# Performance work log

Hardware: AMD Instinct MI355X
Metric: run time of the kernel (lower is better)

## Reference

```python
import jax, jax.numpy as jnp
import numpy as np
from jax import lax

# Model dims (see init_kwargs / mamba_ssm defaults)
B_, L_, D_IN = 8, 512, 128
D_MODEL, N_LAYERS = 512, 2
EXPAND, D_STATE, D_CONV = 2, 16, 4
D_INNER = EXPAND * D_MODEL          # 1024
DT_RANK = (D_MODEL + 15) // 16      # 32


def setup_inputs() -> dict:
    key = jax.random.key(0)
    ks = iter(jax.random.split(key, 32))
    def p(shape, scale=0.02):
        return jax.random.normal(next(ks), shape, jnp.float32) * scale
    inp = {}
    inp["x"] = jax.random.normal(next(ks), (B_, L_, D_IN), jnp.float32)
    # input projection (Linear(input_dim, d_model), with bias)
    inp["proj_in_w"] = p((D_MODEL, D_IN))
    inp["proj_in_b"] = p((D_MODEL,))
    # stacked per-layer Mamba params (leading dim = N_LAYERS)
    inp["in_proj_w"] = p((N_LAYERS, 2 * D_INNER, D_MODEL))      # no bias (mamba default)
    inp["conv_w"]    = p((N_LAYERS, D_INNER, D_CONV))           # depthwise conv1d
    inp["conv_b"]    = p((N_LAYERS, D_INNER))
    inp["x_proj_w"]  = p((N_LAYERS, DT_RANK + 2 * D_STATE, D_INNER))
    inp["dt_proj_w"] = p((N_LAYERS, D_INNER, DT_RANK))
    inp["dt_proj_b"] = jnp.full((N_LAYERS, D_INNER), 0.1, jnp.float32)
    inp["A_log"]     = jnp.log(jnp.tile(jnp.arange(1, D_STATE + 1, dtype=jnp.float32), (N_LAYERS, D_INNER, 1)))
    inp["Dm"]        = jnp.ones((N_LAYERS, D_INNER), jnp.float32)
    inp["out_proj_w"] = p((N_LAYERS, D_MODEL, D_INNER))         # no bias
    # classifier head: Linear(d_model, 64) -> ReLU -> Linear(64, 1)
    inp["cls_w1"] = p((64, D_MODEL)); inp["cls_b1"] = p((64,))
    inp["cls_w2"] = p((1, 64));       inp["cls_b2"] = p((1,))
    return inp


def _mamba_block(h, in_w, cw, cb, xp_w, dt_w, dt_b, A_log, Dm, out_w):
    B, L, _ = h.shape
    xz = jnp.einsum('bld,ed->ble', h, in_w)           # (B, L, 2*d_inner)
    xi, z = jnp.split(xz, 2, axis=-1)
    # causal depthwise conv1d (pad left d_conv-1, crop to L)
    xc = xi.transpose(0, 2, 1)                         # (B, d_inner, L)
    xc = lax.conv_general_dilated(
        xc, cw[:, None, :], (1,), [(D_CONV - 1, 0)],
        feature_group_count=D_INNER,
        dimension_numbers=('NCH', 'OIH', 'NCH')) + cb[None, :, None]
    xc = jax.nn.silu(xc).transpose(0, 2, 1)            # (B, L, d_inner)
    x_dbl = jnp.einsum('bld,ed->ble', xc, xp_w)        # (B, L, dt_rank + 2*d_state)
    dt, Bm, Cm = jnp.split(x_dbl, [DT_RANK, DT_RANK + D_STATE], axis=-1)
    dt = jax.nn.softplus(jnp.einsum('blr,dr->bld', dt, dt_w) + dt_b)  # (B, L, d_inner)
    A = -jnp.exp(A_log)                                # (d_inner, d_state)

    def step(hst, ins):
        dt_t, B_t, C_t, x_t = ins                      # (B,di),(B,ds),(B,ds),(B,di)
        dA = jnp.exp(dt_t[..., None] * A)              # (B, di, ds)
        hst = dA * hst + (dt_t * x_t)[..., None] * B_t[:, None, :]
        y = jnp.einsum('bds,bs->bd', hst, C_t)
        return hst, y

    h0 = jnp.zeros((B, D_INNER, D_STATE), h.dtype)
    xs = (dt.transpose(1, 0, 2), Bm.transpose(1, 0, 2),
          Cm.transpose(1, 0, 2), xc.transpose(1, 0, 2))
    _, ys = lax.scan(step, h0, xs)                     # ys: (L, B, d_inner)
    y = ys.transpose(1, 0, 2) + xc * Dm                # skip term D*x
    y = y * jax.nn.silu(z)                             # gate
    return jnp.einsum('ble,de->bld', y, out_w)         # (B, L, d_model)


def reference(x, proj_in_w, proj_in_b, in_proj_w, conv_w, conv_b, x_proj_w,
              dt_proj_w, dt_proj_b, A_log, Dm, out_proj_w,
              cls_w1, cls_b1, cls_w2, cls_b2):
    h = jnp.einsum('bli,di->bld', x, proj_in_w) + proj_in_b
    for l in range(N_LAYERS):
        h = _mamba_block(h, in_proj_w[l], conv_w[l], conv_b[l], x_proj_w[l],
                         dt_proj_w[l], dt_proj_b[l], A_log[l], Dm[l], out_proj_w[l])
    h = h.mean(axis=1)                                 # (B, d_model); dropout = identity (eval)
    h = jax.nn.relu(h @ cls_w1.T + cls_b1)
    logits = (h @ cls_w2.T + cls_b2).squeeze(-1)       # (B,)
    return logits
```

## Files before the change

### kernel.cpp

```cpp
#include <hip/hip_runtime.h>
#include <hip/hip_bf16.h>

#define B_   8
#define L_   512
#define DIN  128
#define DM   512
#define NLAY 2
#define DI   1024
#define DS   16
#define DTR  32
#define BL   (B_ * L_)
#define KS   8
#define CL   64

typedef short bf16x8 __attribute__((ext_vector_type(8)));
typedef float floatx4 __attribute__((ext_vector_type(4)));

__device__ __forceinline__ unsigned short f2bf(float f) {
    unsigned int u = __float_as_uint(f);
    unsigned int r = (u + 0x7FFF + ((u >> 16) & 1)) >> 16;
    return (unsigned short)r;
}

__global__ __launch_bounds__(256) void cvt_all(
    const float* __restrict__ x,  unsigned short* __restrict__ xbf,
    const float* __restrict__ pw, unsigned short* __restrict__ wpin,
    const float* __restrict__ iw, unsigned short* __restrict__ win,
    const float* __restrict__ ow, unsigned short* __restrict__ wout)
{
    int bid = blockIdx.x;
    const float* src; unsigned short* dst; int off;
    if      (bid < 256)  { src = x;  dst = xbf;  off = bid; }
    else if (bid < 288)  { src = pw; dst = wpin; off = bid - 256; }
    else if (bid < 1312) { src = iw; dst = win;  off = bid - 288; }
    else                 { src = ow; dst = wout; off = bid - 1312; }
    int i = (off * 256 + threadIdx.x) * 8;
    float4 a = *(const float4*)(src + i);
    float4 b = *(const float4*)(src + i + 4);
    unsigned short o[8];
    o[0] = f2bf(a.x); o[1] = f2bf(a.y); o[2] = f2bf(a.z); o[3] = f2bf(a.w);
    o[4] = f2bf(b.x); o[5] = f2bf(b.y); o[6] = f2bf(b.z); o[7] = f2bf(b.w);
    *(uint4*)(dst + i) = *(uint4*)o;
}

__global__ __launch_bounds__(256) void gemm_mfma(
    const unsigned short* __restrict__ A,
    const unsigned short* __restrict__ W,
    const float* __restrict__ bias,
    float* __restrict__ C, unsigned short* __restrict__ Cb,
    int N, int K)
{
    __shared__ unsigned short As[128 * 40];
    __shared__ unsigned short Ws[128 * 40];

    const int tid  = threadIdx.x;
    const int row  = tid >> 1;
    const int half = tid & 1;
    const long aBase = (long)(blockIdx.y * 128 + row) * K + half * 16;
    const long wBase = (long)(blockIdx.x * 128 + row) * K + half * 16;
    const int  lbase = row * 40 + half * 16;

    const int lane = tid & 63;
    const int wv   = tid >> 6;
    const int wm   = (wv >> 1) * 64;
    const int wn   = (wv & 1) * 64;
    const int lr   = lane & 15;
    const int q    = lane >> 4;

    floatx4 acc[4][4];
#pragma unroll
    for (int i = 0; i < 4; ++i)
#pragma unroll
        for (int j = 0; j < 4; ++j)
#pragma unroll
            for (int r = 0; r < 4; ++r) acc[i][j][r] = 0.f;

    for (int k0 = 0; k0 < K; k0 += 32) {
        __syncthreads();
        const unsigned short* ap = A + aBase + k0;
        const unsigned short* wp = W + wBase + k0;
        uint4 a0 = *(const uint4*)ap;
        uint4 a1 = *(const uint4*)(ap + 8);
        uint4 w0 = *(const uint4*)wp;
        uint4 w1 = *(const uint4*)(wp + 8);
        *(uint4*)(As + lbase)     = a0;
        *(uint4*)(As + lbase + 8) = a1;
        *(uint4*)(Ws + lbase)     = w0;
        *(uint4*)(Ws + lbase + 8) = w1;
        __syncthreads();

        bf16x8 af[4], bfr[4];
#pragma unroll
        for (int i = 0; i < 4; ++i)
            af[i] = *(const bf16x8*)(As + (wm + i * 16 + lr) * 40 + q * 8);
#pragma unroll
        for (int j = 0; j < 4; ++j)
            bfr[j] = *(const bf16x8*)(Ws + (wn + j * 16 + lr) * 40 + q * 8);
#pragma unroll
        for (int i = 0; i < 4; ++i)
#pragma unroll
            for (int j = 0; j < 4; ++j)
                acc[i][j] = __builtin_amdgcn_mfma_f32_16x16x32_bf16(
                    af[i], bfr[j], acc[i][j], 0, 0, 0);
    }

#pragma unroll
    for (int i = 0; i < 4; ++i) {
#pragma unroll
        for (int r = 0; r < 4; ++r) {
            const int  crow = blockIdx.y * 128 + wm + i * 16 + q * 4 + r;
            const long base = (long)crow * N + blockIdx.x * 128 + wn + lr;
#pragma unroll
            for (int j = 0; j < 4; ++j) {
                float v = acc[i][j][r];
                C[base + j * 16] = v;
                if (Cb) Cb[base + j * 16] = f2bf(v);
            }
        }
    }
}

__global__ __launch_bounds__(256) void gemm_mfma_n64(
    const unsigned short* __restrict__ A,
    const unsigned short* __restrict__ W,
    const float* __restrict__ bias,
    float* __restrict__ C, unsigned short* __restrict__ Cb,
    int N, int K)
{
    __shared__ unsigned short As[128 * 40];
    __shared__ unsigned short Ws[64 * 40];

    const int tid   = threadIdx.x;
    const int arow  = tid >> 1;
    const int ahalf = tid & 1;
    const long aBase = (long)(blockIdx.y * 128 + arow) * K + ahalf * 16;
    const int  albase = arow * 40 + ahalf * 16;
    const int wrow = tid >> 2;
    const int wq   = tid & 3;
    const long wBase = (long)(blockIdx.x * 64 + wrow) * K + wq * 8;
    const int  wlbase = wrow * 40 + wq * 8;

    const int lane = tid & 63;
    const int wv   = tid >> 6;
    const int wm   = wv * 32;
    const int lr   = lane & 15;
    const int q    = lane >> 4;

    floatx4 acc[2][4];
#pragma unroll
    for (int i = 0; i < 2; ++i)
#pragma unroll
        for (int j = 0; j < 4; ++j)
#pragma unroll
            for (int r = 0; r < 4; ++r) acc[i][j][r] = 0.f;

    for (int k0 = 0; k0 < K; k0 += 32) {
        __syncthreads();
        const unsigned short* ap = A + aBase + k0;
        uint4 a0 = *(const uint4*)ap;
        uint4 a1 = *(const uint4*)(ap + 8);
        uint4 w0 = *(const uint4*)(W + wBase + k0);
        *(uint4*)(As + albase)     = a0;
        *(uint4*)(As + albase + 8) = a1;
        *(uint4*)(Ws + wlbase)     = w0;
        __syncthreads();

        bf16x8 af[2], bfr[4];
#pragma unroll
        for (int i = 0; i < 2; ++i)
            af[i] = *(const bf16x8*)(As + (wm + i * 16 + lr) * 40 + q * 8);
#pragma unroll
        for (int j = 0; j < 4; ++j)
            bfr[j] = *(const bf16x8*)(Ws + (j * 16 + lr) * 40 + q * 8);
#pragma unroll
        for (int i = 0; i < 2; ++i)
#pragma unroll
            for (int j = 0; j < 4; ++j)
                acc[i][j] = __builtin_amdgcn_mfma_f32_16x16x32_bf16(
                    af[i], bfr[j], acc[i][j], 0, 0, 0);
    }

    float bj[4] = {0.f, 0.f, 0.f, 0.f};
    if (bias) {
#pragma unroll
        for (int j = 0; j < 4; ++j)
            bj[j] = bias[blockIdx.x * 64 + j * 16 + lr];
    }
#pragma unroll
    for (int i = 0; i < 2; ++i) {
#pragma unroll
        for (int r = 0; r < 4; ++r) {
            const int  crow = blockIdx.y * 128 + wm + i * 16 + q * 4 + r;
            const long base = (long)crow * N + blockIdx.x * 64 + lr;
#pragma unroll
            for (int j = 0; j < 4; ++j) {
                float v = acc[i][j][r] + bj[j];
                C[base + j * 16] = v;
                if (Cb) Cb[base + j * 16] = f2bf(v);
            }
        }
    }
}

__global__ __launch_bounds__(256) void xproj_partial(
    const float* __restrict__ A, const float* __restrict__ W,
    float* __restrict__ P)
{
    __shared__ float As[16][68];
    __shared__ float Ws[16][68];

    const int tid  = threadIdx.x;
    const int tx   = tid & 15;
    const int ty   = tid >> 4;
    const int lrow = tid >> 2;
    const int lk   = (tid & 3) << 2;
    const int kbase = blockIdx.x * (DI / KS);

    const float* Ap = A + (blockIdx.y * 64 + lrow) * DI + kbase + lk;
    const float* Wp = W + lrow * DI + kbase + lk;

    float acc[4][4] = {};

    for (int k0 = 0; k0 < DI / KS; k0 += 16) {
        float4 av = *(const float4*)(Ap + k0);
        float4 wv = *(const float4*)(Wp + k0);
        __syncthreads();
        As[lk + 0][lrow] = av.x; As[lk + 1][lrow] = av.y;
        As[lk + 2][lrow] = av.z; As[lk + 3][lrow] = av.w;
        Ws[lk + 0][lrow] = wv.x; Ws[lk + 1][lrow] = wv.y;
        Ws[lk + 2][lrow] = wv.z; Ws[lk + 3][lrow] = wv.w;
        __syncthreads();
#pragma unroll
        for (int k = 0; k < 16; ++k) {
            const float4 a4 = *(const float4*)&As[k][ty << 2];
            const float4 w4 = *(const float4*)&Ws[k][tx << 2];
            acc[0][0] += a4.x * w4.x; acc[0][1] += a4.x * w4.y;
            acc[0][2] += a4.x * w4.z; acc[0][3] += a4.x * w4.w;
            acc[1][0] += a4.y * w4.x; acc[1][1] += a4.y * w4.y;
            acc[1][2] += a4.y * w4.z; acc[1][3] += a4.y * w4.w;
            acc[2][0] += a4.z * w4.x; acc[2][1] += a4.z * w4.y;
            acc[2][2] += a4.z * w4.z; acc[2][3] += a4.z * w4.w;
            acc[3][0] += a4.w * w4.x; acc[3][1] += a4.w * w4.y;
            acc[3][2] += a4.w * w4.z; acc[3][3] += a4.w * w4.w;
        }
    }

    float* out = P + (long)blockIdx.x * (BL * 64)
               + (blockIdx.y * 64 + (ty << 2)) * 64 + (tx << 2);
#pragma unroll
    for (int i = 0; i < 4; ++i)
        *(float4*)(out + i * 64) = make_float4(acc[i][0], acc[i][1],
                                               acc[i][2], acc[i][3]);
}

__global__ __launch_bounds__(256) void xproj_reduce(
    const float* __restrict__ P, float* __restrict__ xdbl)
{
    int i = (blockIdx.x * 256 + threadIdx.x) * 4;
    float4 s = *(const float4*)(P + i);
#pragma unroll
    for (int k = 1; k < KS; ++k) {
        float4 p = *(const float4*)(P + (long)k * (BL * 64) + i);
        s.x += p.x; s.y += p.y; s.z += p.z; s.w += p.w;
    }
    *(float4*)(xdbl + i) = s;
}

__global__ __launch_bounds__(256) void conv_silu(
    const float* __restrict__ xz, const float* __restrict__ cw,
    const float* __restrict__ cb, float* __restrict__ xc)
{
    int idx = blockIdx.x * 256 + threadIdx.x;
    int d  = idx & (DI - 1);
    int bl = idx >> 10;
    int t  = bl & (L_ - 1);
    int base = (bl - t) * (2 * DI) + d;
    float acc = cb[d];
    const float* w = cw + d * 4;
    if (t >= 3) {
        acc += w[0] * xz[base + (t - 3) * (2 * DI)];
        acc += w[1] * xz[base + (t - 2) * (2 * DI)];
        acc += w[2] * xz[base + (t - 1) * (2 * DI)];
        acc += w[3] * xz[base + t * (2 * DI)];
    } else {
#pragma unroll
        for (int j = 0; j < 4; ++j) {
            int tt = t - 3 + j;
            if (tt >= 0) acc += w[j] * xz[base + tt * (2 * DI)];
        }
    }
    xc[idx] = acc / (1.f + __expf(-acc));
}

template <int CTRL>
__device__ __forceinline__ float dpp_shr_add(float v) {
    int sh = __builtin_amdgcn_update_dpp(0, __float_as_int(v), CTRL, 0xF, 0xF, true);
    return v + __int_as_float(sh);
}

__global__ __launch_bounds__(256) void scan_fused(
    const float* __restrict__ xc, const float* __restrict__ xdbl,
    const float* __restrict__ A_log, const float* __restrict__ dtw,
    const float* __restrict__ dtpb, const float* __restrict__ Dm,
    const float* __restrict__ xz, unsigned short* __restrict__ ysb16)
{
    __shared__ float  sdtw[16][36];
    __shared__ float  sxd [CL][36];
    __shared__ float2 sdx [CL][17];
    __shared__ float2 sbc [CL][17];
    __shared__ float  sy  [16][68];

    const int tid  = threadIdx.x;
    const int s    = tid & 15;
    const int grp  = tid >> 4;
    const int bd0  = blockIdx.x * 16;
    const int b    = bd0 >> 10;
    const int d0   = bd0 & (DI - 1);
    const int mb0  = b * L_;

    const int j  = tid & 15;
    const int tt = tid >> 4;

    {
        float2 w = *(const float2*)(dtw + (d0 + j) * DTR + tt * 2);
        sdtw[j][tt * 2] = w.x; sdtw[j][tt * 2 + 1] = w.y;
    }
    const float a    = -__expf(A_log[(d0 + grp) * DS + s]);
    const float bias = dtpb[d0 + j];
    const float dmv  = Dm[d0 + j];

    float  rxc[4], rB[4], rC[4], rz[4];
    float2 rxd[4];

#pragma unroll
    for (int i = 0; i < 4; ++i) {
        int m = mb0 + tt + 16 * i;
        rxc[i] = xc[m * DI + d0 + j];
        rxd[i] = *(const float2*)(xdbl + m * 64 + j * 2);
        rB[i]  = xdbl[m * 64 + DTR + j];
        rC[i]  = xdbl[m * 64 + DTR + DS + j];
        rz[i]  = xz[m * (2 * DI) + DI + d0 + j];
    }

    float state = 0.f;

    for (int c = 0; c < L_ / CL; ++c) {
        const int mbase = mb0 + c * CL;

        __syncthreads();
#pragma unroll
        for (int i = 0; i < 4; ++i) {
            int t = tt + 16 * i;
            sdx[t][j].y = rxc[i];
            sxd[t][j * 2]     = rxd[i].x;
            sxd[t][j * 2 + 1] = rxd[i].y;
            sbc[t][j] = make_float2(rB[i], rC[i]);
        }
        __syncthreads();

        float zcur[4];
#pragma unroll
        for (int i = 0; i < 4; ++i) zcur[i] = rz[i];

        if (c < L_ / CL - 1) {
#pragma unroll
            for (int i = 0; i < 4; ++i) {
                int m = mbase + CL + tt + 16 * i;
                rxc[i] = xc[m * DI + d0 + j];
                rxd[i] = *(const float2*)(xdbl + m * 64 + j * 2);
                rB[i]  = xdbl[m * 64 + DTR + j];
                rC[i]  = xdbl[m * 64 + DTR + DS + j];
                rz[i]  = xz[m * (2 * DI) + DI + d0 + j];
            }
        }

        {
            float4 wreg[8];
#pragma unroll
            for (int k = 0; k < 8; ++k) wreg[k] = *(const float4*)&sdtw[j][k * 4];
#pragma unroll
            for (int i = 0; i < 4; ++i) {
                int t = tt + 16 * i;
                float acc = bias;
#pragma unroll
                for (int k = 0; k < 8; ++k) {
                    float4 xv = *(const float4*)&sxd[t][k * 4];
                    acc += xv.x * wreg[k].x + xv.y * wreg[k].y
                         + xv.z * wreg[k].z + xv.w * wreg[k].w;
                }
                sdx[t][j].x = (acc > 20.f) ? acc : __logf(1.f + __expf(acc));
            }
        }
        __syncthreads();

        for (int t4 = 0; t4 < CL; t4 += 4) {
            float ybuf[4];
#pragma unroll
            for (int u = 0; u < 4; ++u) {
                const int t = t4 + u;
                const float2 dx = sdx[t][grp];
                const float2 bc = sbc[t][s];
                const float dA = __expf(dx.x * a);
                state = fmaf(dA, state, dx.x * dx.y * bc.x);
                float contrib = state * bc.y;
                contrib = dpp_shr_add<0x111>(contrib);
                contrib = dpp_shr_add<0x112>(contrib);
                contrib = dpp_shr_add<0x114>(contrib);
                contrib = dpp_shr_add<0x118>(contrib);
                ybuf[u] = contrib;
            }
            if (s == 15) *(float4*)&sy[grp][t4] = *(float4*)ybuf;
        }
        __syncthreads();

#pragma unroll
        for (int i = 0; i < 4; ++i) {
            int t = tt + 16 * i;
            float z = zcur[i];
            float sz = z / (1.f + __expf(-z));
            float val = (sy[j][t] + sdx[t][j].y * dmv) * sz;
            ysb16[(mbase + t) * DI + d0 + j] = f2bf(val);
        }
    }
}

__global__ __launch_bounds__(512) void mean_partial(
    const float* __restrict__ h, float* __restrict__ hmp)
{
    int b = blockIdx.x >> 3, sl = blockIdx.x & 7, d = threadIdx.x;
    float acc = 0.f;
    int t0 = sl * 64;
    for (int t = 0; t < 64; ++t) acc += h[(b * L_ + t0 + t) * DM + d];
    hmp[blockIdx.x * DM + d] = acc;
}

__global__ __launch_bounds__(512) void meancls_kernel(
    const float* __restrict__ hmp, const float* __restrict__ w1,
    const float* __restrict__ b1, const float* __restrict__ w2,
    const float* __restrict__ b2, float* __restrict__ out)
{
    __shared__ float shm[DM];
    __shared__ float su[64];
    const int b = blockIdx.x, tid = threadIdx.x;
    float acc = 0.f;
#pragma unroll
    for (int sl = 0; sl < 8; ++sl) acc += hmp[(b * 8 + sl) * DM + tid];
    shm[tid] = acc * (1.f / (float)L_);
    __syncthreads();

    const int j = tid >> 3, sl = tid & 7;
    const float* wr = w1 + j * DM + sl * 64;
    const float* hb = shm + sl * 64;
    float p = 0.f;
    for (int k = 0; k < 64; k += 4)
        p += hb[k] * wr[k] + hb[k+1] * wr[k+1]
           + hb[k+2] * wr[k+2] + hb[k+3] * wr[k+3];
    p += __shfl_xor(p, 1);
    p += __shfl_xor(p, 2);
    p += __shfl_xor(p, 4);
    if (sl == 0) su[j] = fmaxf(p + b1[j], 0.f) * w2[j];
    __syncthreads();
    if (tid < 64) {
        float v = su[tid];
#pragma unroll
        for (int off = 32; off; off >>= 1) v += __shfl_down(v, off);
        if (tid == 0) out[b] = v + b2[0];
    }
}

extern "C" void kernel_launch(void* const* d_in, const int* in_sizes, int n_in,
                              void* d_out, int out_size, void* d_ws, size_t ws_size,
                              hipStream_t stream) {
    const float* x          = (const float*)d_in[0];
    const float* proj_in_w  = (const float*)d_in[1];
    const float* proj_in_b  = (const float*)d_in[2];
    const float* in_proj_w  = (const float*)d_in[3];
    const float* conv_w     = (const float*)d_in[4];
    const float* conv_b     = (const float*)d_in[5];
    const float* x_proj_w   = (const float*)d_in[6];
    const float* dt_proj_w  = (const float*)d_in[7];
    const float* dt_proj_b  = (const float*)d_in[8];
    const float* A_log      = (const float*)d_in[9];
    const float* Dm         = (const float*)d_in[10];
    const float* out_proj_w = (const float*)d_in[11];
    const float* cls_w1     = (const float*)d_in[12];
    const float* cls_b1     = (const float*)d_in[13];
    const float* cls_w2     = (const float*)d_in[14];
    const float* cls_b2     = (const float*)d_in[15];
    float* out = (float*)d_out;

    float* ws   = (float*)d_ws;
    float* h    = ws;
    float* xz   = h    + BL * DM;
    float* xcb  = xz   + BL * 2 * DI;
    float* xdbl = xcb  + BL * DI;
    float* scr  = xdbl + BL * 64;
    float* hm   = scr  + 2 * BL * DI;
    float* hmp  = hm   + B_ * DM;
    unsigned short* u16  = (unsigned short*)(hmp + 64 * DM);
    unsigned short* xbf  = u16;
    unsigned short* hbf  = xbf  + BL * DIN;
    unsigned short* ysbf = hbf  + BL * DM;
    unsigned short* wpin = ysbf + BL * DI;
    unsigned short* win  = wpin + DM * DIN;
    unsigned short* wout = win  + NLAY * 2 * DI * DM;
    float* xpart = scr;

    cvt_all<<<1824, 256, 0, stream>>>(x, xbf, proj_in_w, wpin,
                                      in_proj_w, win, out_proj_w, wout);

    gemm_mfma_n64<<<dim3(DM / 64, BL / 128), 256, 0, stream>>>(
        xbf, wpin, proj_in_b, h, hbf, DM, DIN);

    for (int l = 0; l < NLAY; ++l) {
        gemm_mfma<<<dim3(2 * DI / 128, BL / 128), 256, 0, stream>>>(
            hbf, win + l * 2 * DI * DM, nullptr, xz, nullptr, 2 * DI, DM);
        conv_silu<<<(BL * DI) / 256, 256, 0, stream>>>(
            xz, conv_w + l * DI * 4, conv_b + l * DI, xcb);
        xproj_partial<<<dim3(KS, BL / 64), 256, 0, stream>>>(
            xcb, x_proj_w + l * 64 * DI, xpart);
        xproj_reduce<<<(BL * 64) / 1024, 256, 0, stream>>>(xpart, xdbl);
        scan_fused<<<(B_ * DI) / 16, 256, 0, stream>>>(
            xcb, xdbl, A_log + l * DI * DS, dt_proj_w + l * DI * DTR,
            dt_proj_b + l * DI, Dm + l * DI, xz, ysbf);
        gemm_mfma_n64<<<dim3(DM / 64, BL / 128), 256, 0, stream>>>(
            ysbf, wout + l * DM * DI, nullptr, h, hbf, DM, DI);
    }

    mean_partial<<<B_ * 8, DM, 0, stream>>>(h, hmp);
    meancls_kernel<<<B_, 512, 0, stream>>>(hmp, cls_w1, cls_b1,
                                           cls_w2, cls_b2, out);
}
```

Baseline: 367.9 us.

## Fuse conv+SiLU into x_proj, store xz as bf16, widen scan chunk

Measured after the change: 351.3 us. 1.05x faster.

```diff
diff --git a/kernel.cpp b/kernel.cpp
--- a/kernel.cpp
+++ b/kernel.cpp
@@ -11,7 +11,8 @@
 #define DTR  32
 #define BL   (B_ * L_)
 #define KS   8
-#define CL   64
+#define CL   128
+#define NCH  (L_ / CL)
 
 typedef short bf16x8 __attribute__((ext_vector_type(8)));
 typedef float floatx4 __attribute__((ext_vector_type(4)));
@@ -21,6 +22,15 @@
     unsigned int r = (u + 0x7FFF + ((u >> 16) & 1)) >> 16;
     return (unsigned short)r;
 }
+__device__ __forceinline__ float bf2f(unsigned short u) {
+    return __uint_as_float((unsigned int)u << 16);
+}
+
+#if __has_builtin(__builtin_amdgcn_exp2f)
+#define EXP2(x) __builtin_amdgcn_exp2f(x)
+#else
+#define EXP2(x) __expf((x) * 0.69314718056f)
+#endif
 
 __global__ __launch_bounds__(256) void cvt_all(
     const float* __restrict__ x,  unsigned short* __restrict__ xbf,
@@ -46,7 +56,6 @@
 __global__ __launch_bounds__(256) void gemm_mfma(
     const unsigned short* __restrict__ A,
     const unsigned short* __restrict__ W,
-    const float* __restrict__ bias,
     float* __restrict__ C, unsigned short* __restrict__ Cb,
     int N, int K)
 {
@@ -113,7 +122,7 @@
 #pragma unroll
             for (int j = 0; j < 4; ++j) {
                 float v = acc[i][j][r];
-                C[base + j * 16] = v;
+                if (C)  C[base + j * 16] = v;
                 if (Cb) Cb[base + j * 16] = f2bf(v);
             }
         }
@@ -195,16 +204,17 @@
 #pragma unroll
             for (int j = 0; j < 4; ++j) {
                 float v = acc[i][j][r] + bj[j];
-                C[base + j * 16] = v;
+                if (C)  C[base + j * 16] = v;
                 if (Cb) Cb[base + j * 16] = f2bf(v);
             }
         }
     }
 }
 
-__global__ __launch_bounds__(256) void xproj_partial(
-    const float* __restrict__ A, const float* __restrict__ W,
-    float* __restrict__ P)
+__global__ __launch_bounds__(256) void xprojconv(
+    const unsigned short* __restrict__ xzb, const float* __restrict__ cw,
+    const float* __restrict__ cb, const float* __restrict__ W,
+    float* __restrict__ P, float* __restrict__ xcout)
 {
     __shared__ float As[16][68];
     __shared__ float Ws[16][68];
@@ -216,32 +226,59 @@
     const int lk   = (tid & 3) << 2;
     const int kbase = blockIdx.x * (DI / KS);
 
-    const float* Ap = A + (blockIdx.y * 64 + lrow) * DI + kbase + lk;
+    const int m = blockIdx.y * 64 + lrow;
+    const int t = m & (L_ - 1);
     const float* Wp = W + lrow * DI + kbase + lk;
 
     float acc[4][4] = {};
 
     for (int k0 = 0; k0 < DI / KS; k0 += 16) {
-        float4 av = *(const float4*)(Ap + k0);
+        const int dcol = kbase + k0 + lk;
+        float4 cbv = *(const float4*)(cb + dcol);
+        float sums[4] = {cbv.x, cbv.y, cbv.z, cbv.w};
+        float4 cwq[4];
+#pragma unroll
+        for (int q = 0; q < 4; ++q) cwq[q] = *(const float4*)(cw + (dcol + q) * 4);
+#pragma unroll
+        for (int w = 0; w < 4; ++w) {
+            int tw = t - 3 + w;
+            if (tw >= 0) {
+                const uint2 up = *(const uint2*)(xzb + (long)(m - 3 + w) * (2 * DI) + dcol);
+                float x0 = __uint_as_float(up.x << 16);
+                float x1 = __uint_as_float(up.x & 0xffff0000u);
+                float x2 = __uint_as_float(up.y << 16);
+                float x3 = __uint_as_float(up.y & 0xffff0000u);
+                sums[0] += ((const float*)&cwq[0])[w] * x0;
+                sums[1] += ((const float*)&cwq[1])[w] * x1;
+                sums[2] += ((const float*)&cwq[2])[w] * x2;
+                sums[3] += ((const float*)&cwq[3])[w] * x3;
+            }
+        }
+        float4 a4;
+#pragma unroll
+        for (int q = 0; q < 4; ++q)
+            ((float*)&a4)[q] = sums[q] / (1.f + __expf(-sums[q]));
         float4 wv = *(const float4*)(Wp + k0);
-        __syncthreads();
-        As[lk + 0][lrow] = av.x; As[lk + 1][lrow] = av.y;
-        As[lk + 2][lrow] = av.z; As[lk + 3][lrow] = av.w;
+        *(float4*)(xcout + (long)m * DI + dcol) = a4;
+
+        __syncthreads();
+        As[lk + 0][lrow] = a4.x; As[lk + 1][lrow] = a4.y;
+        As[lk + 2][lrow] = a4.z; As[lk + 3][lrow] = a4.w;
         Ws[lk + 0][lrow] = wv.x; Ws[lk + 1][lrow] = wv.y;
         Ws[lk + 2][lrow] = wv.z; Ws[lk + 3][lrow] = wv.w;
         __syncthreads();
 #pragma unroll
         for (int k = 0; k < 16; ++k) {
-            const float4 a4 = *(const float4*)&As[k][ty << 2];
-            const float4 w4 = *(const float4*)&Ws[k][tx << 2];
-            acc[0][0] += a4.x * w4.x; acc[0][1] += a4.x * w4.y;
-            acc[0][2] += a4.x * w4.z; acc[0][3] += a4.x * w4.w;
-            acc[1][0] += a4.y * w4.x; acc[1][1] += a4.y * w4.y;
-            acc[1][2] += a4.y * w4.z; acc[1][3] += a4.y * w4.w;
-            acc[2][0] += a4.z * w4.x; acc[2][1] += a4.z * w4.y;
-            acc[2][2] += a4.z * w4.z; acc[2][3] += a4.z * w4.w;
-            acc[3][0] += a4.w * w4.x; acc[3][1] += a4.w * w4.y;
-            acc[3][2] += a4.w * w4.z; acc[3][3] += a4.w * w4.w;
+            const float4 a44 = *(const float4*)&As[k][ty << 2];
+            const float4 w4  = *(const float4*)&Ws[k][tx << 2];
+            acc[0][0] += a44.x * w4.x; acc[0][1] += a44.x * w4.y;
+            acc[0][2] += a44.x * w4.z; acc[0][3] += a44.x * w4.w;
+            acc[1][0] += a44.y * w4.x; acc[1][1] += a44.y * w4.y;
+            acc[1][2] += a44.y * w4.z; acc[1][3] += a44.y * w4.w;
+            acc[2][0] += a44.z * w4.x; acc[2][1] += a44.z * w4.y;
+            acc[2][2] += a44.z * w4.z; acc[2][3] += a44.z * w4.w;
+            acc[3][0] += a44.w * w4.x; acc[3][1] += a44.w * w4.y;
+            acc[3][2] += a44.w * w4.z; acc[3][3] += a44.w * w4.w;
         }
     }
 
@@ -264,32 +301,6 @@
         s.x += p.x; s.y += p.y; s.z += p.z; s.w += p.w;
     }
     *(float4*)(xdbl + i) = s;
-}
-
-__global__ __launch_bounds__(256) void conv_silu(
-    const float* __restrict__ xz, const float* __restrict__ cw,
-    const float* __restrict__ cb, float* __restrict__ xc)
-{
-    int idx = blockIdx.x * 256 + threadIdx.x;
-    int d  = idx & (DI - 1);
-    int bl = idx >> 10;
-    int t  = bl & (L_ - 1);
-    int base = (bl - t) * (2 * DI) + d;
-    float acc = cb[d];
-    const float* w = cw + d * 4;
-    if (t >= 3) {
-        acc += w[0] * xz[base + (t - 3) * (2 * DI)];
-        acc += w[1] * xz[base + (t - 2) * (2 * DI)];
-        acc += w[2] * xz[base + (t - 1) * (2 * DI)];
-        acc += w[3] * xz[base + t * (2 * DI)];
-    } else {
-#pragma unroll
-        for (int j = 0; j < 4; ++j) {
-            int tt = t - 3 + j;
-            if (tt >= 0) acc += w[j] * xz[base + tt * (2 * DI)];
-        }
-    }
-    xc[idx] = acc / (1.f + __expf(-acc));
 }
 
 template <int CTRL>
@@ -302,13 +313,13 @@
     const float* __restrict__ xc, const float* __restrict__ xdbl,
     const float* __restrict__ A_log, const float* __restrict__ dtw,
     const float* __restrict__ dtpb, const float* __restrict__ Dm,
-    const float* __restrict__ xz, unsigned short* __restrict__ ysb16)
+    const unsigned short* __restrict__ xzb, unsigned short* __restrict__ ysb16)
 {
     __shared__ float  sdtw[16][36];
     __shared__ float  sxd [CL][36];
-    __shared__ float2 sdx [CL][17];
-    __shared__ float2 sbc [CL][17];
-    __shared__ float  sy  [16][68];
+    __shared__ float4 sdp [CL / 2][17];
+    __shared__ float4 sbc4[CL / 2][17];
+    __shared__ float  sy  [16][CL + 4];
 
     const int tid  = threadIdx.x;
     const int s    = tid & 15;
@@ -329,48 +340,44 @@
     const float bias = dtpb[d0 + j];
     const float dmv  = Dm[d0 + j];
 
-    float  rxc[4], rB[4], rC[4], rz[4];
-    float2 rxd[4];
-
-#pragma unroll
-    for (int i = 0; i < 4; ++i) {
+    float  rxc[8], rB[8], rC[8], rz[8];
+    float2 rxd[8];
+#pragma unroll
+    for (int i = 0; i < 8; ++i) {
         int m = mb0 + tt + 16 * i;
         rxc[i] = xc[m * DI + d0 + j];
         rxd[i] = *(const float2*)(xdbl + m * 64 + j * 2);
         rB[i]  = xdbl[m * 64 + DTR + j];
         rC[i]  = xdbl[m * 64 + DTR + DS + j];
-        rz[i]  = xz[m * (2 * DI) + DI + d0 + j];
+        rz[i]  = bf2f(xzb[(long)m * (2 * DI) + DI + d0 + j]);
     }
 
     float state = 0.f;
 
-    for (int c = 0; c < L_ / CL; ++c) {
+    for (int c = 0; c < NCH; ++c) {
         const int mbase = mb0 + c * CL;
-
-        __syncthreads();
-#pragma unroll
-        for (int i = 0; i < 4; ++i) {
+        float xcur[8], zcur[8];
+#pragma unroll
+        for (int i = 0; i < 8; ++i) { xcur[i] = rxc[i]; zcur[i] = rz[i]; }
+
+        __syncthreads();
+#pragma unroll
+        for (int i = 0; i < 8; ++i) {
             int t = tt + 16 * i;
-            sdx[t][j].y = rxc[i];
-            sxd[t][j * 2]     = rxd[i].x;
-            sxd[t][j * 2 + 1] = rxd[i].y;
-            sbc[t][j] = make_float2(rB[i], rC[i]);
-        }
-        __syncthreads();
-
-        float zcur[4];
-#pragma unroll
-        for (int i = 0; i < 4; ++i) zcur[i] = rz[i];
-
-        if (c < L_ / CL - 1) {
-#pragma unroll
-            for (int i = 0; i < 4; ++i) {
+            *(float2*)&sxd[t][j * 2] = rxd[i];
+            ((float2*)&sbc4[t >> 1][j])[t & 1] = make_float2(rB[i], rC[i]);
+        }
+        __syncthreads();
+
+        if (c < NCH - 1) {
+#pragma unroll
+            for (int i = 0; i < 8; ++i) {
                 int m = mbase + CL + tt + 16 * i;
                 rxc[i] = xc[m * DI + d0 + j];
                 rxd[i] = *(const float2*)(xdbl + m * 64 + j * 2);
                 rB[i]  = xdbl[m * 64 + DTR + j];
                 rC[i]  = xdbl[m * 64 + DTR + DS + j];
-                rz[i]  = xz[m * (2 * DI) + DI + d0 + j];
+                rz[i]  = bf2f(xzb[(long)m * (2 * DI) + DI + d0 + j]);
             }
         }
 
@@ -379,7 +386,7 @@
 #pragma unroll
             for (int k = 0; k < 8; ++k) wreg[k] = *(const float4*)&sdtw[j][k * 4];
 #pragma unroll
-            for (int i = 0; i < 4; ++i) {
+            for (int i = 0; i < 8; ++i) {
                 int t = tt + 16 * i;
                 float acc = bias;
 #pragma unroll
@@ -388,7 +395,9 @@
                     acc += xv.x * wreg[k].x + xv.y * wreg[k].y
                          + xv.z * wreg[k].z + xv.w * wreg[k].w;
                 }
-                sdx[t][j].x = (acc > 20.f) ? acc : __logf(1.f + __expf(acc));
+                float dt = (acc > 20.f) ? acc : __logf(1.f + __expf(acc));
+                ((float2*)&sdp[t >> 1][j])[t & 1] =
+                    make_float2(dt * 1.44269504f, dt * xcur[i]);
             }
         }
         __syncthreads();
@@ -396,29 +405,41 @@
         for (int t4 = 0; t4 < CL; t4 += 4) {
             float ybuf[4];
 #pragma unroll
-            for (int u = 0; u < 4; ++u) {
-                const int t = t4 + u;
-                const float2 dx = sdx[t][grp];
-                const float2 bc = sbc[t][s];
-                const float dA = __expf(dx.x * a);
-                state = fmaf(dA, state, dx.x * dx.y * bc.x);
-                float contrib = state * bc.y;
-                contrib = dpp_shr_add<0x111>(contrib);
-                contrib = dpp_shr_add<0x112>(contrib);
-                contrib = dpp_shr_add<0x114>(contrib);
-                contrib = dpp_shr_add<0x118>(contrib);
-                ybuf[u] = contrib;
+            for (int h = 0; h < 2; ++h) {
+                const int t2 = (t4 >> 1) + h;
+                const float4 dp = sdp[t2][grp];
+                const float4 bc = sbc4[t2][s];
+                {
+                    const float dA = EXP2(dp.x * a);
+                    state = fmaf(dA, state, dp.y * bc.x);
+                    float contrib = state * bc.y;
+                    contrib = dpp_shr_add<0x111>(contrib);
+                    contrib = dpp_shr_add<0x112>(contrib);
+                    contrib = dpp_shr_add<0x114>(contrib);
+                    contrib = dpp_shr_add<0x118>(contrib);
+                    ybuf[h * 2] = contrib;
+                }
+                {
+                    const float dA = EXP2(dp.z * a);
+                    state = fmaf(dA, state, dp.w * bc.z);
+                    float contrib = state * bc.w;
+                    contrib = dpp_shr_add<0x111>(contrib);
+                    contrib = dpp_shr_add<0x112>(contrib);
+                    contrib = dpp_shr_add<0x114>(contrib);
+                    contrib = dpp_shr_add<0x118>(contrib);
+                    ybuf[h * 2 + 1] = contrib;
+                }
             }
             if (s == 15) *(float4*)&sy[grp][t4] = *(float4*)ybuf;
         }
         __syncthreads();
 
 #pragma unroll
-        for (int i = 0; i < 4; ++i) {
+        for (int i = 0; i < 8; ++i) {
             int t = tt + 16 * i;
             float z = zcur[i];
             float sz = z / (1.f + __expf(-z));
-            float val = (sy[j][t] + sdx[t][j].y * dmv) * sz;
+            float val = (sy[j][t] + xcur[i] * dmv) * sz;
             ysb16[(mbase + t) * DI + d0 + j] = f2bf(val);
         }
     }
@@ -491,12 +512,13 @@
 
     float* ws   = (float*)d_ws;
     float* h    = ws;
-    float* xz   = h    + BL * DM;
-    float* xcb  = xz   + BL * 2 * DI;
+    float* xzf  = h    + BL * DM;
+    float* xcb  = xzf  + BL * 2 * DI;
     float* xdbl = xcb  + BL * DI;
     float* scr  = xdbl + BL * 64;
     float* hm   = scr  + 2 * BL * DI;
     float* hmp  = hm   + B_ * DM;
+    unsigned short* xzb  = (unsigned short*)xzf;
     unsigned short* u16  = (unsigned short*)(hmp + 64 * DM);
     unsigned short* xbf  = u16;
     unsigned short* hbf  = xbf  + BL * DIN;
@@ -514,15 +536,14 @@
 
     for (int l = 0; l < NLAY; ++l) {
         gemm_mfma<<<dim3(2 * DI / 128, BL / 128), 256, 0, stream>>>(
-            hbf, win + l * 2 * DI * DM, nullptr, xz, nullptr, 2 * DI, DM);
-        conv_silu<<<(BL * DI) / 256, 256, 0, stream>>>(
-            xz, conv_w + l * DI * 4, conv_b + l * DI, xcb);
-        xproj_partial<<<dim3(KS, BL / 64), 256, 0, stream>>>(
-            xcb, x_proj_w + l * 64 * DI, xpart);
+            hbf, win + l * 2 * DI * DM, nullptr, xzb, 2 * DI, DM);
+        xprojconv<<<dim3(KS, BL / 64), 256, 0, stream>>>(
+            xzb, conv_w + l * DI * 4, conv_b + l * DI,
+            x_proj_w + l * 64 * DI, xpart, xcb);
         xproj_reduce<<<(BL * 64) / 1024, 256, 0, stream>>>(xpart, xdbl);
         scan_fused<<<(B_ * DI) / 16, 256, 0, stream>>>(
             xcb, xdbl, A_log + l * DI * DS, dt_proj_w + l * DI * DTR,
-            dt_proj_b + l * DI, Dm + l * DI, xz, ysbf);
+            dt_proj_b + l * DI, Dm + l * DI, xzb, ysbf);
         gemm_mfma_n64<<<dim3(DM / 64, BL / 128), 256, 0, stream>>>(
             ysbf, wout + l * DM * DI, nullptr, h, hbf, DM, DI);
     }
```
